# Optimization experiments

Measured on AMD Instinct MI355X. Metric: run time of the kernel, lower is better.

Reference implementation:

```python
import jax, jax.numpy as jnp
import numpy as np

B, N, D, H = 4, 4096, 128, 8
DH = D // H
EPS = 1e-6


def _layernorm(x, g, b):
    mu = jnp.mean(x, axis=-1, keepdims=True)
    var = jnp.var(x, axis=-1, keepdims=True)
    return (x - mu) * jax.lax.rsqrt(var + EPS) * g + b


def setup_inputs() -> dict:
    key = jax.random.key(0)
    ks = jax.random.split(key, 12)
    p = lambda k, shape: (jax.random.normal(k, shape, jnp.float32) * 0.02)
    x = jax.random.normal(ks[0], (B, N, D), jnp.float32)
    # scale fx so the sigmoid of the N-length contraction is not fully saturated
    fx = jax.random.normal(ks[1], (B, N, D), jnp.float32) / N
    return {
        "x": x,
        "fx": fx,
        "ln1_g": jnp.ones((D,), jnp.float32),
        "ln1_b": jnp.zeros((D,), jnp.float32),
        "wq": p(ks[2], (D, D)),
        "wk": p(ks[3], (D, D)),
        "wv": p(ks[4], (D, D)),
        "wo": p(ks[5], (D, D)),
        "bo": jnp.zeros((D,), jnp.float32),
        "ln2_g": jnp.ones((D,), jnp.float32),
        "ln2_b": jnp.zeros((D,), jnp.float32),
        "w1": p(ks[6], (D, D)),
        "b1": jnp.zeros((D,), jnp.float32),
        "w2": p(ks[7], (D, D)),
        "b2": jnp.zeros((D,), jnp.float32),
    }


def reference(x, fx, ln1_g, ln1_b, wq, wk, wv, wo, bo, ln2_g, ln2_b, w1, b1, w2, b2):
    b, n, d = x.shape
    h, dh = H, d // H
    # --- pre-norm linear self-attention ---
    xn = _layernorm(x, ln1_g, ln1_b)
    def heads(w):  # [b,n,d] @ w^T -> [b,h,n,dh]
        return jnp.einsum('bnd,ed->bne', xn, w).reshape(b, n, h, dh).transpose(0, 2, 1, 3)
    q = jax.nn.softmax(heads(wq), axis=-1)   # softmax over feature dim
    k = jax.nn.softmax(heads(wk), axis=2)    # softmax over sequence dim
    v = heads(wv)
    ctx = jnp.einsum('bhnd,bhne->bhde', k, v)         # [b,h,dh,dh]
    attn = jnp.einsum('bhnd,bhde->bhne', q, ctx)       # [b,h,n,dh]
    attn = attn.transpose(0, 2, 1, 3).reshape(b, n, d)
    attn = jnp.einsum('bnd,ed->bne', attn, wo) + bo
    x = x + attn                                       # residual (dropout=identity)
    # --- pre-norm MLP ---
    y = _layernorm(x, ln2_g, ln2_b)
    y = jax.nn.gelu(jnp.einsum('bnd,ed->bne', y, w1) + b1, approximate=False)
    y = jnp.einsum('bnd,ed->bne', y, w2) + b2
    x = x + y
    # --- quadratic update: sigmoid((x x^T) fx), as written in the module ---
    gram = jnp.einsum('bnd,bmd->bnm', x, x)            # [b,n,n] materialized, faithful
    fx = jax.nn.sigmoid(jnp.einsum('bnm,bmd->bnd', gram, fx))
    return (x, fx)
```

## Files before the change

### kernel.cpp

```cpp
#include <hip/hip_runtime.h>
#include <math.h>

#define BB 4
#define NN 4096
#define DD 128
#define MM (BB*NN)

typedef __attribute__((ext_vector_type(8))) short short8;
typedef __attribute__((ext_vector_type(4))) float f32x4;

__device__ inline short f2bf(float f) {
    unsigned u = __float_as_uint(f);
    u = (u + 0x7FFFu + ((u >> 16) & 1u)) >> 16;
    return (short)u;
}
__device__ inline float bf2f(short s) {
    return __uint_as_float(((unsigned)(unsigned short)s) << 16);
}
__device__ inline short8 pack_bf8(float4 a, float4 b) {
    short8 o;
    o[0] = f2bf(a.x); o[1] = f2bf(a.y); o[2] = f2bf(a.z); o[3] = f2bf(a.w);
    o[4] = f2bf(b.x); o[5] = f2bf(b.y); o[6] = f2bf(b.z); o[7] = f2bf(b.w);
    return o;
}
__device__ inline int swzoff(int row, int col) {
    return ((row * 128 + col) * 2) ^ ((row & 7) << 4);
}

__global__ __launch_bounds__(256) void wprep(const float* __restrict__ w0, const float* __restrict__ w1,
                                             const float* __restrict__ w2, const float* __restrict__ w3,
                                             const float* __restrict__ w4, short* __restrict__ wf) {
    int m = blockIdx.x >> 3;
    int j = (blockIdx.x & 7) * 256 + threadIdx.x;
    const float* W = (m == 0) ? w0 : (m == 1) ? w1 : (m == 2) ? w2 : (m == 3) ? w3 : w4;
    int nt = j >> 8, ks = (j >> 6) & 3, l = j & 63, r = l & 15, g = l >> 4;
    const float* src = W + (size_t)(nt * 16 + r) * DD + 32 * ks + 8 * g;
    float4 a = *(const float4*)src;
    float4 b = *(const float4*)(src + 4);
    ((short8*)(wf + (size_t)m * 16384))[j] = pack_bf8(a, b);
}

__global__ __launch_bounds__(256) void lnctx(const float* __restrict__ x,
                                             const float* __restrict__ lng,
                                             const float* __restrict__ lnb,
                                             const short* __restrict__ wf,
                                             float* __restrict__ partC,
                                             float* __restrict__ pcs) {
    __shared__ float ekL[32][132];
    __shared__ float vL[32][132];
    int t = threadIdx.x;
    int block_row = blockIdx.x * 32;
    int w = t >> 6, l = t & 63, r = l & 15, g = l >> 4;
    int rh = w >> 1, nt0 = (w & 1) << 2;
    int row0 = block_row + rh * 16;

    const float* ap = x + (size_t)(row0 + r) * DD + 8 * g;
    float4 av0[4], av1[4];
    #pragma unroll
    for (int ks = 0; ks < 4; ks++) {
        av0[ks] = *(const float4*)(ap + 32 * ks);
        av1[ks] = *(const float4*)(ap + 32 * ks + 4);
    }
    float s = 0.f, ss = 0.f;
    #pragma unroll
    for (int ks = 0; ks < 4; ks++) {
        float4 a = av0[ks], b = av1[ks];
        s  += a.x + a.y + a.z + a.w + b.x + b.y + b.z + b.w;
        ss += a.x*a.x + a.y*a.y + a.z*a.z + a.w*a.w + b.x*b.x + b.y*b.y + b.z*b.z + b.w*b.w;
    }
    s  += __shfl_xor(s, 16);  s  += __shfl_xor(s, 32);
    ss += __shfl_xor(ss, 16); ss += __shfl_xor(ss, 32);
    float mu = s * (1.0f / DD);
    float var = ss * (1.0f / DD) - mu * mu;
    float rs = rsqrtf(var + 1e-6f);

    short8 af[4];
    #pragma unroll
    for (int ks = 0; ks < 4; ks++) {
        float4 g0 = *(const float4*)(lng + 32 * ks + 8 * g);
        float4 g1 = *(const float4*)(lng + 32 * ks + 8 * g + 4);
        float4 b0 = *(const float4*)(lnb + 32 * ks + 8 * g);
        float4 b1 = *(const float4*)(lnb + 32 * ks + 8 * g + 4);
        float4 n0, n1;
        n0.x = (av0[ks].x - mu) * rs * g0.x + b0.x;
        n0.y = (av0[ks].y - mu) * rs * g0.y + b0.y;
        n0.z = (av0[ks].z - mu) * rs * g0.z + b0.z;
        n0.w = (av0[ks].w - mu) * rs * g0.w + b0.w;
        n1.x = (av1[ks].x - mu) * rs * g1.x + b1.x;
        n1.y = (av1[ks].y - mu) * rs * g1.y + b1.y;
        n1.z = (av1[ks].z - mu) * rs * g1.z + b1.z;
        n1.w = (av1[ks].w - mu) * rs * g1.w + b1.w;
        af[ks] = pack_bf8(n0, n1);
    }

    f32x4 acc[2][4];
    #pragma unroll
    for (int m = 0; m < 2; m++)
        #pragma unroll
        for (int n = 0; n < 4; n++) acc[m][n] = (f32x4){0.f, 0.f, 0.f, 0.f};
    const short8* wp8 = (const short8*)wf;
    #pragma unroll
    for (int ks = 0; ks < 4; ks++)
        #pragma unroll
        for (int m = 0; m < 2; m++)
            #pragma unroll
            for (int n = 0; n < 4; n++)
                acc[m][n] = __builtin_amdgcn_mfma_f32_16x16x32_bf16(
                    af[ks], wp8[(size_t)m * 2048 + ((nt0 + n) * 4 + ks) * 64 + l], acc[m][n], 0, 0, 0);

    #pragma unroll
    for (int n = 0; n < 4; n++) {
        int col = (nt0 + n) * 16 + r;
        #pragma unroll
        for (int j = 0; j < 4; j++) {
            int rowL = rh * 16 + 4 * g + j;
            ekL[rowL][col] = __expf(acc[0][n][j]);
            vL[rowL][col]  = acc[1][n][j];
        }
    }
    __syncthreads();

    int h = t >> 5, sub = t & 31, d = sub >> 1, e0 = (sub & 1) * 8;
    float cs = 0.f;
    float sc[8] = {0.f, 0.f, 0.f, 0.f, 0.f, 0.f, 0.f, 0.f};
    #pragma unroll 8
    for (int row = 0; row < 32; row++) {
        float ekv = ekL[row][h * 16 + d];
        float4 v0 = *(const float4*)&vL[row][h * 16 + e0];
        float4 v1 = *(const float4*)&vL[row][h * 16 + e0 + 4];
        sc[0] += ekv * v0.x; sc[1] += ekv * v0.y; sc[2] += ekv * v0.z; sc[3] += ekv * v0.w;
        sc[4] += ekv * v1.x; sc[5] += ekv * v1.y; sc[6] += ekv * v1.z; sc[7] += ekv * v1.w;
        cs += ekv;
    }
    float* cb = partC + (size_t)blockIdx.x * 2048 + h * 256 + d * 16 + e0;
    *(float4*)cb       = (float4){sc[0], sc[1], sc[2], sc[3]};
    *(float4*)(cb + 4) = (float4){sc[4], sc[5], sc[6], sc[7]};
    if ((sub & 1) == 0) pcs[(size_t)blockIdx.x * 128 + h * 16 + d] = cs;
}

__global__ __launch_bounds__(256) void ctxred(const float* __restrict__ part,
                                              float* __restrict__ ctxacc) {
    int k = blockIdx.x;
    int b = k >> 4, s0 = (k & 15) * 128;
    int t = threadIdx.x;
    int slot = s0 + (t & 127), half = t >> 7;
    float s = 0.f;
    #pragma unroll 8
    for (int c = half * 64; c < half * 64 + 64; c++)
        s += part[(size_t)((b << 7) + c) * 2048 + slot];
    __shared__ float red[128];
    if (half) red[t & 127] = s;
    __syncthreads();
    if (!half) ctxacc[(size_t)b * 2048 + slot] = s + red[t & 127];
}

__global__ __launch_bounds__(256) void build_mt_k(const float* __restrict__ ctxacc,
                                                  const float* __restrict__ pcs,
                                                  const float* __restrict__ wo,
                                                  short* __restrict__ mtfrag) {
    int b = blockIdx.x >> 3, nt = blockIdx.x & 7;
    int t = threadIdx.x;
    __shared__ float ctxL[2048];
    __shared__ float csL[128];
    __shared__ float woL[2048];
    #pragma unroll
    for (int i = 0; i < 8; i++) {
        int idx = i * 256 + t;
        ctxL[idx] = ctxacc[(size_t)b * 2048 + idx];
        woL[idx]  = wo[(size_t)(nt * 16) * DD + idx];
    }
    if (t < 128) {
        float s = 0.f;
        #pragma unroll 8
        for (int c = 0; c < 128; c++) s += pcs[(size_t)(b * 128 + c) * 128 + t];
        csL[t] = s;
    }
    __syncthreads();
    int ks = (t >> 6) & 3, l = t & 63, r = l & 15, g = l >> 4;
    short8 o;
    #pragma unroll
    for (int i2 = 0; i2 < 8; i2++) {
        int k = 32 * ks + 8 * g + i2;
        float inv = 1.0f / csL[k];
        const float* wrow = woL + r * DD + (k >> 4) * 16;
        float s = 0.f;
        #pragma unroll
        for (int eo = 0; eo < 16; eo++) s += ctxL[k * 16 + eo] * wrow[eo];
        o[i2] = f2bf(s * inv);
    }
    ((short8*)(mtfrag + (size_t)b * 16384))[nt * 256 + t] = o;
}

__global__ __launch_bounds__(256) void fused_mid(const float* __restrict__ x,
                                                 const float* __restrict__ ln1g,
                                                 const float* __restrict__ ln1b,
                                                 const short* __restrict__ wqf,
                                                 const short* __restrict__ mtf,
                                                 const float* __restrict__ bo,
                                                 const float* __restrict__ ln2g,
                                                 const float* __restrict__ ln2b,
                                                 const short* __restrict__ w1f,
                                                 const float* __restrict__ b1,
                                                 const short* __restrict__ w2f,
                                                 const float* __restrict__ b2,
                                                 float* __restrict__ xfinal,
                                                 short* __restrict__ xbf) {
    __shared__ __align__(16) char ex[32 * 128 * 2];
    __shared__ float ex2f[32][132];
    __shared__ float redS[4][16], redSS[4][16];
    int t = threadIdx.x;
    int block_row = blockIdx.x * 32;
    int w = t >> 6, l = t & 63, r = l & 15, g = l >> 4;
    int rh = w >> 1, nt0 = (w & 1) << 2;
    int row0 = block_row + rh * 16;
    int rrow = rh * 16 + r;

    const float* ap = x + (size_t)(row0 + r) * DD + 8 * g;
    float4 av0[4], av1[4];
    #pragma unroll
    for (int ks = 0; ks < 4; ks++) {
        av0[ks] = *(const float4*)(ap + 32 * ks);
        av1[ks] = *(const float4*)(ap + 32 * ks + 4);
    }
    if ((w & 1) == 0) {
        #pragma unroll
        for (int ks = 0; ks < 4; ks++) {
            *(float4*)&ex2f[rrow][32 * ks + 8 * g]     = av0[ks];
            *(float4*)&ex2f[rrow][32 * ks + 8 * g + 4] = av1[ks];
        }
    }
    float s = 0.f, ss = 0.f;
    #pragma unroll
    for (int ks = 0; ks < 4; ks++) {
        float4 a = av0[ks], b = av1[ks];
        s  += a.x + a.y + a.z + a.w + b.x + b.y + b.z + b.w;
        ss += a.x*a.x + a.y*a.y + a.z*a.z + a.w*a.w + b.x*b.x + b.y*b.y + b.z*b.z + b.w*b.w;
    }
    s  += __shfl_xor(s, 16);  s  += __shfl_xor(s, 32);
    ss += __shfl_xor(ss, 16); ss += __shfl_xor(ss, 32);
    float mu1 = s * (1.0f / DD);
    float var1 = ss * (1.0f / DD) - mu1 * mu1;
    float rs1 = rsqrtf(var1 + 1e-6f);
    short8 af[4];
    #pragma unroll
    for (int ks = 0; ks < 4; ks++) {
        float4 g0 = *(const float4*)(ln1g + 32 * ks + 8 * g);
        float4 g1 = *(const float4*)(ln1g + 32 * ks + 8 * g + 4);
        float4 b0 = *(const float4*)(ln1b + 32 * ks + 8 * g);
        float4 b1v = *(const float4*)(ln1b + 32 * ks + 8 * g + 4);
        float4 n0, n1;
        n0.x = (av0[ks].x - mu1) * rs1 * g0.x + b0.x;
        n0.y = (av0[ks].y - mu1) * rs1 * g0.y + b0.y;
        n0.z = (av0[ks].z - mu1) * rs1 * g0.z + b0.z;
        n0.w = (av0[ks].w - mu1) * rs1 * g0.w + b0.w;
        n1.x = (av1[ks].x - mu1) * rs1 * g1.x + b1v.x;
        n1.y = (av1[ks].y - mu1) * rs1 * g1.y + b1v.y;
        n1.z = (av1[ks].z - mu1) * rs1 * g1.z + b1v.z;
        n1.w = (av1[ks].w - mu1) * rs1 * g1.w + b1v.w;
        af[ks] = pack_bf8(n0, n1);
    }

    const short8* qp = (const short8*)wqf;
    f32x4 accq[4];
    #pragma unroll
    for (int n = 0; n < 4; n++) accq[n] = (f32x4){0.f, 0.f, 0.f, 0.f};
    #pragma unroll
    for (int ks = 0; ks < 4; ks++)
        #pragma unroll
        for (int n = 0; n < 4; n++)
            accq[n] = __builtin_amdgcn_mfma_f32_16x16x32_bf16(
                af[ks], qp[((nt0 + n) * 4 + ks) * 64 + l], accq[n], 0, 0, 0);
    #pragma unroll
    for (int n = 0; n < 4; n++) {
        int col = (nt0 + n) * 16 + r;
        #pragma unroll
        for (int j = 0; j < 4; j++) {
            float e = __expf(accq[n][j]);
            float sm = e;
            sm += __shfl_xor(sm, 1); sm += __shfl_xor(sm, 2);
            sm += __shfl_xor(sm, 4); sm += __shfl_xor(sm, 8);
            *(short*)(ex + swzoff(rh * 16 + 4 * g + j, col)) = f2bf(e / sm);
        }
    }
    __syncthreads();

    short8 qf[4];
    #pragma unroll
    for (int ks = 0; ks < 4; ks++)
        qf[ks] = *(const short8*)(ex + swzoff(rrow, 32 * ks + 8 * g));
    float xres[4][4];
    #pragma unroll
    for (int n = 0; n < 4; n++)
        #pragma unroll
        for (int j = 0; j < 4; j++)
            xres[n][j] = ex2f[rh * 16 + 4 * g + j][(nt0 + n) * 16 + r];

    const short8* mp = (const short8*)(mtf + (size_t)(block_row >> 12) * 16384);
    f32x4 acc[4];
    #pragma unroll
    for (int n = 0; n < 4; n++) acc[n] = (f32x4){0.f, 0.f, 0.f, 0.f};
    #pragma unroll
    for (int ks = 0; ks < 4; ks++)
        #pragma unroll
        for (int n = 0; n < 4; n++)
            acc[n] = __builtin_amdgcn_mfma_f32_16x16x32_bf16(
                qf[ks], mp[((nt0 + n) * 4 + ks) * 64 + l], acc[n], 0, 0, 0);

    float vv[4][4];
    #pragma unroll
    for (int n = 0; n < 4; n++) {
        int col = (nt0 + n) * 16 + r;
        float bv = bo[col];
        #pragma unroll
        for (int j = 0; j < 4; j++)
            vv[n][j] = acc[n][j] + bv + xres[n][j];
    }

    #pragma unroll
    for (int j = 0; j < 4; j++) {
        float s1  = vv[0][j] + vv[1][j] + vv[2][j] + vv[3][j];
        float s2 = vv[0][j]*vv[0][j] + vv[1][j]*vv[1][j] + vv[2][j]*vv[2][j] + vv[3][j]*vv[3][j];
        s1 += __shfl_xor(s1, 1); s1 += __shfl_xor(s1, 2); s1 += __shfl_xor(s1, 4); s1 += __shfl_xor(s1, 8);
        s2 += __shfl_xor(s2, 1); s2 += __shfl_xor(s2, 2); s2 += __shfl_xor(s2, 4); s2 += __shfl_xor(s2, 8);
        if (r == 0) { redS[w][4 * g + j] = s1; redSS[w][4 * g + j] = s2; }
    }
    __syncthreads();
    int base = w & 2;
    #pragma unroll
    for (int j = 0; j < 4; j++) {
        int rr = 4 * g + j;
        float S  = redS[base][rr]  + redS[base + 1][rr];
        float SS = redSS[base][rr] + redSS[base + 1][rr];
        float mu = S * (1.0f / DD);
        float var = SS * (1.0f / DD) - mu * mu;
        float rs = rsqrtf(var + 1e-6f);
        int rowL = rh * 16 + rr;
        #pragma unroll
        for (int n = 0; n < 4; n++) {
            int col = (nt0 + n) * 16 + r;
            float y = (vv[n][j] - mu) * rs * ln2g[col] + ln2b[col];
            *(short*)(ex + swzoff(rowL, col)) = f2bf(y);
        }
    }
    __syncthreads();
    short8 yf[4];
    #pragma unroll
    for (int ks = 0; ks < 4; ks++)
        yf[ks] = *(const short8*)(ex + swzoff(rrow, 32 * ks + 8 * g));
    __syncthreads();
    const short8* w1p = (const short8*)w1f;
    f32x4 acc2[4];
    #pragma unroll
    for (int n = 0; n < 4; n++) acc2[n] = (f32x4){0.f, 0.f, 0.f, 0.f};
    #pragma unroll
    for (int ks = 0; ks < 4; ks++)
        #pragma unroll
        for (int n = 0; n < 4; n++)
            acc2[n] = __builtin_amdgcn_mfma_f32_16x16x32_bf16(
                yf[ks], w1p[((nt0 + n) * 4 + ks) * 64 + l], acc2[n], 0, 0, 0);
    #pragma unroll
    for (int n = 0; n < 4; n++) {
        int col = (nt0 + n) * 16 + r;
        float bv = b1[col];
        #pragma unroll
        for (int j = 0; j < 4; j++) {
            float v = acc2[n][j] + bv;
            v = 0.5f * v * (1.0f + erff(v * 0.70710678118654752f));
            *(short*)(ex + swzoff(rh * 16 + 4 * g + j, col)) = f2bf(v);
        }
    }
    __syncthreads();
    short8 hf[4];
    #pragma unroll
    for (int ks = 0; ks < 4; ks++)
        hf[ks] = *(const short8*)(ex + swzoff(rrow, 32 * ks + 8 * g));
    const short8* w2p = (const short8*)w2f;
    f32x4 acc3[4];
    #pragma unroll
    for (int n = 0; n < 4; n++) acc3[n] = (f32x4){0.f, 0.f, 0.f, 0.f};
    #pragma unroll
    for (int ks = 0; ks < 4; ks++)
        #pragma unroll
        for (int n = 0; n < 4; n++)
            acc3[n] = __builtin_amdgcn_mfma_f32_16x16x32_bf16(
                hf[ks], w2p[((nt0 + n) * 4 + ks) * 64 + l], acc3[n], 0, 0, 0);
    #pragma unroll
    for (int n = 0; n < 4; n++) {
        int col = (nt0 + n) * 16 + r;
        float bv = b2[col];
        #pragma unroll
        for (int j = 0; j < 4; j++) {
            float v = acc3[n][j] + bv + vv[n][j];
            size_t row = (size_t)(row0 + 4 * g + j);
            xfinal[row * DD + col] = v;
            xbf[row * DD + col] = f2bf(v);
        }
    }
}

__global__ __launch_bounds__(512) void sbuild_p(const short* __restrict__ xf,
                                                const float* __restrict__ fx,
                                                short* __restrict__ part) {
    int b = blockIdx.x >> 6, chunk = blockIdx.x & 63;
    int t = threadIdx.x;
    __shared__ float xs[64 * 128], fs[64 * 128];
    const short* xb = xf + ((size_t)b * NN + chunk * 64) * DD;
    const float* fb = fx + ((size_t)b * NN + chunk * 64) * DD;
    const short8* xg = (const short8*)xb;
    float4* xs4 = (float4*)xs; float4* fs4 = (float4*)fs;
    const float4* fg = (const float4*)fb;
    #pragma unroll
    for (int i = 0; i < 2; i++) {
        int j = i * 512 + t;
        short8 s8 = xg[j];
        float4 a = {bf2f(s8[0]), bf2f(s8[1]), bf2f(s8[2]), bf2f(s8[3])};
        float4 c = {bf2f(s8[4]), bf2f(s8[5]), bf2f(s8[6]), bf2f(s8[7])};
        xs4[2 * j] = a; xs4[2 * j + 1] = c;
    }
    #pragma unroll
    for (int i = 0; i < 4; i++) {
        int j = i * 512 + t;
        fs4[j] = fg[j];
    }
    __syncthreads();
    int td = t & 15, te = t >> 4;
    float acc[8][4];
    #pragma unroll
    for (int a = 0; a < 8; a++)
        #pragma unroll
        for (int c = 0; c < 4; c++) acc[a][c] = 0.f;
    for (int r = 0; r < 64; r++) {
        float4 x0 = xs4[r * 32 + td * 2], x1 = xs4[r * 32 + td * 2 + 1];
        float4 f0 = fs4[r * 32 + te];
        float xv[8] = {x0.x, x0.y, x0.z, x0.w, x1.x, x1.y, x1.z, x1.w};
        float fv[4] = {f0.x, f0.y, f0.z, f0.w};
        #pragma unroll
        for (int a = 0; a < 8; a++)
            #pragma unroll
            for (int c = 0; c < 4; c++) acc[a][c] = fmaf(xv[a], fv[c], acc[a][c]);
    }
    short* pb = part + (size_t)blockIdx.x * 16384;
    #pragma unroll
    for (int ci = 0; ci < 4; ci++) {
        short8 o;
        #pragma unroll
        for (int a = 0; a < 8; a++) o[a] = f2bf(acc[a][ci]);
        *(short8*)(pb + (size_t)(te * 4 + ci) * 128 + td * 8) = o;
    }
}

__global__ __launch_bounds__(256) void sreduce2(const short* __restrict__ part,
                                                float* __restrict__ S_T) {
    int b = blockIdx.x >> 7, e = blockIdx.x & 127;
    int t = threadIdx.x;
    int d8 = (t & 15) * 8;
    int ch0 = t >> 4;
    float s[8] = {0.f, 0.f, 0.f, 0.f, 0.f, 0.f, 0.f, 0.f};
    #pragma unroll
    for (int cc = 0; cc < 4; cc++) {
        int ch = ch0 + cc * 16;
        short8 u = *(const short8*)(part + (size_t)(b * 64 + ch) * 16384 + e * 128 + d8);
        #pragma unroll
        for (int i = 0; i < 8; i++) s[i] += bf2f(u[i]);
    }
    #pragma unroll
    for (int i = 0; i < 8; i++) {
        s[i] += __shfl_xor(s[i], 16);
        s[i] += __shfl_xor(s[i], 32);
    }
    __shared__ float red[4][128];
    int w = t >> 6;
    if ((t & 63) < 16) {
        #pragma unroll
        for (int i = 0; i < 8; i++) red[w][d8 + i] = s[i];
    }
    __syncthreads();
    if (t < 128)
        S_T[((size_t)b * 128 + e) * 128 + t] = red[0][t] + red[1][t] + red[2][t] + red[3][t];
}

__global__ __launch_bounds__(256) void gemm_sig(const short* __restrict__ A,
                                                const float* __restrict__ S_T,
                                                float* __restrict__ Cf) {
    int t = threadIdx.x;
    int block_row = blockIdx.x * 32;
    int w = t >> 6, l = t & 63, r = l & 15, g = l >> 4;
    int row0 = block_row + ((w >> 1) << 4);
    int nt0 = (w & 1) << 2;
    const short8* ap = (const short8*)(A + (size_t)(row0 + r) * DD + 8 * g);
    short8 af[4];
    #pragma unroll
    for (int ks = 0; ks < 4; ks++) af[ks] = ap[ks * 4];
    const float* sp = S_T + (size_t)(block_row >> 12) * 16384;
    short8 bf[4][4];
    #pragma unroll
    for (int n = 0; n < 4; n++) {
        const float* se = sp + (size_t)((nt0 + n) * 16 + r) * 128 + 8 * g;
        #pragma unroll
        for (int ks = 0; ks < 4; ks++) {
            float4 a = *(const float4*)(se + 32 * ks);
            float4 c = *(const float4*)(se + 32 * ks + 4);
            bf[n][ks] = pack_bf8(a, c);
        }
    }
    f32x4 acc[4];
    #pragma unroll
    for (int n = 0; n < 4; n++) acc[n] = (f32x4){0.f, 0.f, 0.f, 0.f};
    #pragma unroll
    for (int ks = 0; ks < 4; ks++)
        #pragma unroll
        for (int n = 0; n < 4; n++)
            acc[n] = __builtin_amdgcn_mfma_f32_16x16x32_bf16(
                af[ks], bf[n][ks], acc[n], 0, 0, 0);
    #pragma unroll
    for (int n = 0; n < 4; n++) {
        int col = (nt0 + n) * 16 + r;
        #pragma unroll
        for (int j = 0; j < 4; j++) {
            float v = 1.0f / (1.0f + __expf(-acc[n][j]));
            Cf[(size_t)(row0 + 4 * g + j) * DD + col] = v;
        }
    }
}

extern "C" void kernel_launch(void* const* d_in, const int* in_sizes, int n_in,
                              void* d_out, int out_size, void* d_ws, size_t ws_size,
                              hipStream_t stream) {
    const float* x    = (const float*)d_in[0];
    const float* fx   = (const float*)d_in[1];
    const float* ln1g = (const float*)d_in[2];
    const float* ln1b = (const float*)d_in[3];
    const float* wq   = (const float*)d_in[4];
    const float* wk   = (const float*)d_in[5];
    const float* wv   = (const float*)d_in[6];
    const float* wo   = (const float*)d_in[7];
    const float* bo   = (const float*)d_in[8];
    const float* ln2g = (const float*)d_in[9];
    const float* ln2b = (const float*)d_in[10];
    const float* w1   = (const float*)d_in[11];
    const float* b1   = (const float*)d_in[12];
    const float* w2   = (const float*)d_in[13];
    const float* b2   = (const float*)d_in[14];

    float* out = (float*)d_out;
    float* xfinal = out;
    float* fxout  = out + (size_t)MM * DD;

    float* ws = (float*)d_ws;
    short* xbf    = (short*)ws;
    short* partSb = (short*)(ws + 1048576);
    short* wfW    = (short*)(ws + 3145728);
    float* partC  = ws + 3145728 + 40960;
    float* pcs    = partC + 1048576;
    float* ctxacc = pcs + 65536;
    float* S_T    = ctxacc + 8192;
    short* mtf    = (short*)(S_T + 65536);

    wprep<<<40, 256, 0, stream>>>(wq, wk, wv, w1, w2, wfW);
    lnctx<<<512, 256, 0, stream>>>(x, ln1g, ln1b, wfW + 16384, partC, pcs);
    ctxred<<<64, 256, 0, stream>>>(partC, ctxacc);
    build_mt_k<<<32, 256, 0, stream>>>(ctxacc, pcs, wo, mtf);
    fused_mid<<<512, 256, 0, stream>>>(x, ln1g, ln1b, wfW, mtf, bo, ln2g, ln2b,
                                       wfW + 3 * 16384, b1, wfW + 4 * 16384, b2,
                                       xfinal, xbf);
    sbuild_p<<<256, 512, 0, stream>>>(xbf, fx, partSb);
    sreduce2<<<512, 256, 0, stream>>>(partSb, S_T);
    gemm_sig<<<512, 256, 0, stream>>>(xbf, S_T, fxout);
}
```

Before: 73.06 us.

## Halve row tile to 16 rows per block, doubling grid size for lnctx, fused_mid, gemm_sig

Shrinks the per-block row tile from 32 to 16 rows, so each of the four waves now covers two column tiles of the same 16 rows instead of four column tiles of half the rows. Grids double to 1024 blocks to give more parallelism on the large CU count. The partial-context buffers double in size, so ctxred and build_mt_k must reduce twice as many partials. In exchange, weight fragments are reloaded by twice as many blocks and the LayerNorm statistics in fused_mid now need a four-wave cross reduction.

```diff
diff --git a/kernel.cpp b/kernel.cpp
--- a/kernel.cpp
+++ b/kernel.cpp
@@ -46,15 +46,14 @@
                                              const short* __restrict__ wf,
                                              float* __restrict__ partC,
                                              float* __restrict__ pcs) {
-    __shared__ float ekL[32][132];
-    __shared__ float vL[32][132];
-    int t = threadIdx.x;
-    int block_row = blockIdx.x * 32;
+    __shared__ float ekL[16][132];
+    __shared__ float vL[16][132];
+    int t = threadIdx.x;
+    int block_row = blockIdx.x * 16;
     int w = t >> 6, l = t & 63, r = l & 15, g = l >> 4;
-    int rh = w >> 1, nt0 = (w & 1) << 2;
-    int row0 = block_row + rh * 16;
-
-    const float* ap = x + (size_t)(row0 + r) * DD + 8 * g;
+    int nt0 = w << 1;
+
+    const float* ap = x + (size_t)(block_row + r) * DD + 8 * g;
     float4 av0[4], av1[4];
     #pragma unroll
     for (int ks = 0; ks < 4; ks++) {
@@ -93,27 +92,27 @@
         af[ks] = pack_bf8(n0, n1);
     }
 
-    f32x4 acc[2][4];
+    f32x4 acc[2][2];
     #pragma unroll
     for (int m = 0; m < 2; m++)
         #pragma unroll
-        for (int n = 0; n < 4; n++) acc[m][n] = (f32x4){0.f, 0.f, 0.f, 0.f};
+        for (int n = 0; n < 2; n++) acc[m][n] = (f32x4){0.f, 0.f, 0.f, 0.f};
     const short8* wp8 = (const short8*)wf;
     #pragma unroll
     for (int ks = 0; ks < 4; ks++)
         #pragma unroll
         for (int m = 0; m < 2; m++)
             #pragma unroll
-            for (int n = 0; n < 4; n++)
+            for (int n = 0; n < 2; n++)
                 acc[m][n] = __builtin_amdgcn_mfma_f32_16x16x32_bf16(
                     af[ks], wp8[(size_t)m * 2048 + ((nt0 + n) * 4 + ks) * 64 + l], acc[m][n], 0, 0, 0);
 
     #pragma unroll
-    for (int n = 0; n < 4; n++) {
+    for (int n = 0; n < 2; n++) {
         int col = (nt0 + n) * 16 + r;
         #pragma unroll
         for (int j = 0; j < 4; j++) {
-            int rowL = rh * 16 + 4 * g + j;
+            int rowL = 4 * g + j;
             ekL[rowL][col] = __expf(acc[0][n][j]);
             vL[rowL][col]  = acc[1][n][j];
         }
@@ -123,8 +122,8 @@
     int h = t >> 5, sub = t & 31, d = sub >> 1, e0 = (sub & 1) * 8;
     float cs = 0.f;
     float sc[8] = {0.f, 0.f, 0.f, 0.f, 0.f, 0.f, 0.f, 0.f};
-    #pragma unroll 8
-    for (int row = 0; row < 32; row++) {
+    #pragma unroll
+    for (int row = 0; row < 16; row++) {
         float ekv = ekL[row][h * 16 + d];
         float4 v0 = *(const float4*)&vL[row][h * 16 + e0];
         float4 v1 = *(const float4*)&vL[row][h * 16 + e0 + 4];
@@ -146,8 +145,8 @@
     int slot = s0 + (t & 127), half = t >> 7;
     float s = 0.f;
     #pragma unroll 8
-    for (int c = half * 64; c < half * 64 + 64; c++)
-        s += part[(size_t)((b << 7) + c) * 2048 + slot];
+    for (int c = half * 128; c < half * 128 + 128; c++)
+        s += part[(size_t)(b * 256 + c) * 2048 + slot];
     __shared__ float red[128];
     if (half) red[t & 127] = s;
     __syncthreads();
@@ -172,7 +171,7 @@
     if (t < 128) {
         float s = 0.f;
         #pragma unroll 8
-        for (int c = 0; c < 128; c++) s += pcs[(size_t)(b * 128 + c) * 128 + t];
+        for (int c = 0; c < 256; c++) s += pcs[(size_t)(b * 256 + c) * 128 + t];
         csL[t] = s;
     }
     __syncthreads();
@@ -205,28 +204,26 @@
                                                  const float* __restrict__ b2,
                                                  float* __restrict__ xfinal,
                                                  short* __restrict__ xbf) {
-    __shared__ __align__(16) char ex[32 * 128 * 2];
-    __shared__ float ex2f[32][132];
+    __shared__ __align__(16) char ex[16 * 128 * 2];
+    __shared__ float ex2f[16][132];
     __shared__ float redS[4][16], redSS[4][16];
     int t = threadIdx.x;
-    int block_row = blockIdx.x * 32;
+    int block_row = blockIdx.x * 16;
     int w = t >> 6, l = t & 63, r = l & 15, g = l >> 4;
-    int rh = w >> 1, nt0 = (w & 1) << 2;
-    int row0 = block_row + rh * 16;
-    int rrow = rh * 16 + r;
-
-    const float* ap = x + (size_t)(row0 + r) * DD + 8 * g;
+    int nt0 = w << 1;
+
+    const float* ap = x + (size_t)(block_row + r) * DD + 8 * g;
     float4 av0[4], av1[4];
     #pragma unroll
     for (int ks = 0; ks < 4; ks++) {
         av0[ks] = *(const float4*)(ap + 32 * ks);
         av1[ks] = *(const float4*)(ap + 32 * ks + 4);
     }
-    if ((w & 1) == 0) {
+    if (w == 0) {
         #pragma unroll
         for (int ks = 0; ks < 4; ks++) {
-            *(float4*)&ex2f[rrow][32 * ks + 8 * g]     = av0[ks];
-            *(float4*)&ex2f[rrow][32 * ks + 8 * g + 4] = av1[ks];
+            *(float4*)&ex2f[r][32 * ks + 8 * g]     = av0[ks];
+            *(float4*)&ex2f[r][32 * ks + 8 * g + 4] = av1[ks];
         }
     }
     float s = 0.f, ss = 0.f;
@@ -261,17 +258,17 @@
     }
 
     const short8* qp = (const short8*)wqf;
-    f32x4 accq[4];
-    #pragma unroll
-    for (int n = 0; n < 4; n++) accq[n] = (f32x4){0.f, 0.f, 0.f, 0.f};
-    #pragma unroll
-    for (int ks = 0; ks < 4; ks++)
-        #pragma unroll
-        for (int n = 0; n < 4; n++)
+    f32x4 accq[2];
+    #pragma unroll
+    for (int n = 0; n < 2; n++) accq[n] = (f32x4){0.f, 0.f, 0.f, 0.f};
+    #pragma unroll
+    for (int ks = 0; ks < 4; ks++)
+        #pragma unroll
+        for (int n = 0; n < 2; n++)
             accq[n] = __builtin_amdgcn_mfma_f32_16x16x32_bf16(
                 af[ks], qp[((nt0 + n) * 4 + ks) * 64 + l], accq[n], 0, 0, 0);
     #pragma unroll
-    for (int n = 0; n < 4; n++) {
+    for (int n = 0; n < 2; n++) {
         int col = (nt0 + n) * 16 + r;
         #pragma unroll
         for (int j = 0; j < 4; j++) {
@@ -279,7 +276,7 @@
             float sm = e;
             sm += __shfl_xor(sm, 1); sm += __shfl_xor(sm, 2);
             sm += __shfl_xor(sm, 4); sm += __shfl_xor(sm, 8);
-            *(short*)(ex + swzoff(rh * 16 + 4 * g + j, col)) = f2bf(e / sm);
+            *(short*)(ex + swzoff(4 * g + j, col)) = f2bf(e / sm);
         }
     }
     __syncthreads();
@@ -287,28 +284,28 @@
     short8 qf[4];
     #pragma unroll
     for (int ks = 0; ks < 4; ks++)
-        qf[ks] = *(const short8*)(ex + swzoff(rrow, 32 * ks + 8 * g));
-    float xres[4][4];
-    #pragma unroll
-    for (int n = 0; n < 4; n++)
+        qf[ks] = *(const short8*)(ex + swzoff(r, 32 * ks + 8 * g));
+    float xres[2][4];
+    #pragma unroll
+    for (int n = 0; n < 2; n++)
         #pragma unroll
         for (int j = 0; j < 4; j++)
-            xres[n][j] = ex2f[rh * 16 + 4 * g + j][(nt0 + n) * 16 + r];
+            xres[n][j] = ex2f[4 * g + j][(nt0 + n) * 16 + r];
 
     const short8* mp = (const short8*)(mtf + (size_t)(block_row >> 12) * 16384);
-    f32x4 acc[4];
-    #pragma unroll
-    for (int n = 0; n < 4; n++) acc[n] = (f32x4){0.f, 0.f, 0.f, 0.f};
-    #pragma unroll
-    for (int ks = 0; ks < 4; ks++)
-        #pragma unroll
-        for (int n = 0; n < 4; n++)
+    f32x4 acc[2];
+    #pragma unroll
+    for (int n = 0; n < 2; n++) acc[n] = (f32x4){0.f, 0.f, 0.f, 0.f};
+    #pragma unroll
+    for (int ks = 0; ks < 4; ks++)
+        #pragma unroll
+        for (int n = 0; n < 2; n++)
             acc[n] = __builtin_amdgcn_mfma_f32_16x16x32_bf16(
                 qf[ks], mp[((nt0 + n) * 4 + ks) * 64 + l], acc[n], 0, 0, 0);
 
-    float vv[4][4];
-    #pragma unroll
-    for (int n = 0; n < 4; n++) {
+    float vv[2][4];
+    #pragma unroll
+    for (int n = 0; n < 2; n++) {
         int col = (nt0 + n) * 16 + r;
         float bv = bo[col];
         #pragma unroll
@@ -318,80 +315,78 @@
 
     #pragma unroll
     for (int j = 0; j < 4; j++) {
-        float s1  = vv[0][j] + vv[1][j] + vv[2][j] + vv[3][j];
-        float s2 = vv[0][j]*vv[0][j] + vv[1][j]*vv[1][j] + vv[2][j]*vv[2][j] + vv[3][j]*vv[3][j];
+        float s1 = vv[0][j] + vv[1][j];
+        float s2 = vv[0][j]*vv[0][j] + vv[1][j]*vv[1][j];
         s1 += __shfl_xor(s1, 1); s1 += __shfl_xor(s1, 2); s1 += __shfl_xor(s1, 4); s1 += __shfl_xor(s1, 8);
         s2 += __shfl_xor(s2, 1); s2 += __shfl_xor(s2, 2); s2 += __shfl_xor(s2, 4); s2 += __shfl_xor(s2, 8);
         if (r == 0) { redS[w][4 * g + j] = s1; redSS[w][4 * g + j] = s2; }
     }
     __syncthreads();
-    int base = w & 2;
     #pragma unroll
     for (int j = 0; j < 4; j++) {
         int rr = 4 * g + j;
-        float S  = redS[base][rr]  + redS[base + 1][rr];
-        float SS = redSS[base][rr] + redSS[base + 1][rr];
+        float S  = redS[0][rr]  + redS[1][rr]  + redS[2][rr]  + redS[3][rr];
+        float SS = redSS[0][rr] + redSS[1][rr] + redSS[2][rr] + redSS[3][rr];
         float mu = S * (1.0f / DD);
         float var = SS * (1.0f / DD) - mu * mu;
         float rs = rsqrtf(var + 1e-6f);
-        int rowL = rh * 16 + rr;
-        #pragma unroll
-        for (int n = 0; n < 4; n++) {
+        #pragma unroll
+        for (int n = 0; n < 2; n++) {
             int col = (nt0 + n) * 16 + r;
             float y = (vv[n][j] - mu) * rs * ln2g[col] + ln2b[col];
-            *(short*)(ex + swzoff(rowL, col)) = f2bf(y);
+            *(short*)(ex + swzoff(rr, col)) = f2bf(y);
         }
     }
     __syncthreads();
     short8 yf[4];
     #pragma unroll
     for (int ks = 0; ks < 4; ks++)
-        yf[ks] = *(const short8*)(ex + swzoff(rrow, 32 * ks + 8 * g));
+        yf[ks] = *(const short8*)(ex + swzoff(r, 32 * ks + 8 * g));
     __syncthreads();
     const short8* w1p = (const short8*)w1f;
-    f32x4 acc2[4];
-    #pragma unroll
-    for (int n = 0; n < 4; n++) acc2[n] = (f32x4){0.f, 0.f, 0.f, 0.f};
-    #pragma unroll
-    for (int ks = 0; ks < 4; ks++)
-        #pragma unroll
-        for (int n = 0; n < 4; n++)
+    f32x4 acc2[2];
+    #pragma unroll
+    for (int n = 0; n < 2; n++) acc2[n] = (f32x4){0.f, 0.f, 0.f, 0.f};
+    #pragma unroll
+    for (int ks = 0; ks < 4; ks++)
+        #pragma unroll
+        for (int n = 0; n < 2; n++)
             acc2[n] = __builtin_amdgcn_mfma_f32_16x16x32_bf16(
                 yf[ks], w1p[((nt0 + n) * 4 + ks) * 64 + l], acc2[n], 0, 0, 0);
     #pragma unroll
-    for (int n = 0; n < 4; n++) {
+    for (int n = 0; n < 2; n++) {
         int col = (nt0 + n) * 16 + r;
         float bv = b1[col];
         #pragma unroll
         for (int j = 0; j < 4; j++) {
             float v = acc2[n][j] + bv;
             v = 0.5f * v * (1.0f + erff(v * 0.70710678118654752f));
-            *(short*)(ex + swzoff(rh * 16 + 4 * g + j, col)) = f2bf(v);
+            *(short*)(ex + swzoff(4 * g + j, col)) = f2bf(v);
         }
     }
     __syncthreads();
     short8 hf[4];
     #pragma unroll
     for (int ks = 0; ks < 4; ks++)
-        hf[ks] = *(const short8*)(ex + swzoff(rrow, 32 * ks + 8 * g));
+        hf[ks] = *(const short8*)(ex + swzoff(r, 32 * ks + 8 * g));
     const short8* w2p = (const short8*)w2f;
-    f32x4 acc3[4];
-    #pragma unroll
-    for (int n = 0; n < 4; n++) acc3[n] = (f32x4){0.f, 0.f, 0.f, 0.f};
-    #pragma unroll
-    for (int ks = 0; ks < 4; ks++)
-        #pragma unroll
-        for (int n = 0; n < 4; n++)
+    f32x4 acc3[2];
+    #pragma unroll
+    for (int n = 0; n < 2; n++) acc3[n] = (f32x4){0.f, 0.f, 0.f, 0.f};
+    #pragma unroll
+    for (int ks = 0; ks < 4; ks++)
+        #pragma unroll
+        for (int n = 0; n < 2; n++)
             acc3[n] = __builtin_amdgcn_mfma_f32_16x16x32_bf16(
                 hf[ks], w2p[((nt0 + n) * 4 + ks) * 64 + l], acc3[n], 0, 0, 0);
     #pragma unroll
-    for (int n = 0; n < 4; n++) {
+    for (int n = 0; n < 2; n++) {
         int col = (nt0 + n) * 16 + r;
         float bv = b2[col];
         #pragma unroll
         for (int j = 0; j < 4; j++) {
             float v = acc3[n][j] + bv + vv[n][j];
-            size_t row = (size_t)(row0 + 4 * g + j);
+            size_t row = (size_t)(block_row + 4 * g + j);
             xfinal[row * DD + col] = v;
             xbf[row * DD + col] = f2bf(v);
         }
@@ -483,18 +478,17 @@
                                                 const float* __restrict__ S_T,
                                                 float* __restrict__ Cf) {
     int t = threadIdx.x;
-    int block_row = blockIdx.x * 32;
+    int block_row = blockIdx.x * 16;
     int w = t >> 6, l = t & 63, r = l & 15, g = l >> 4;
-    int row0 = block_row + ((w >> 1) << 4);
-    int nt0 = (w & 1) << 2;
-    const short8* ap = (const short8*)(A + (size_t)(row0 + r) * DD + 8 * g);
+    int nt0 = w << 1;
+    const short8* ap = (const short8*)(A + (size_t)(block_row + r) * DD + 8 * g);
     short8 af[4];
     #pragma unroll
     for (int ks = 0; ks < 4; ks++) af[ks] = ap[ks * 4];
     const float* sp = S_T + (size_t)(block_row >> 12) * 16384;
-    short8 bf[4][4];
-    #pragma unroll
-    for (int n = 0; n < 4; n++) {
+    short8 bf[2][4];
+    #pragma unroll
+    for (int n = 0; n < 2; n++) {
         const float* se = sp + (size_t)((nt0 + n) * 16 + r) * 128 + 8 * g;
         #pragma unroll
         for (int ks = 0; ks < 4; ks++) {
@@ -503,22 +497,22 @@
             bf[n][ks] = pack_bf8(a, c);
         }
     }
-    f32x4 acc[4];
-    #pragma unroll
-    for (int n = 0; n < 4; n++) acc[n] = (f32x4){0.f, 0.f, 0.f, 0.f};
-    #pragma unroll
-    for (int ks = 0; ks < 4; ks++)
-        #pragma unroll
-        for (int n = 0; n < 4; n++)
+    f32x4 acc[2];
+    #pragma unroll
+    for (int n = 0; n < 2; n++) acc[n] = (f32x4){0.f, 0.f, 0.f, 0.f};
+    #pragma unroll
+    for (int ks = 0; ks < 4; ks++)
+        #pragma unroll
+        for (int n = 0; n < 2; n++)
             acc[n] = __builtin_amdgcn_mfma_f32_16x16x32_bf16(
                 af[ks], bf[n][ks], acc[n], 0, 0, 0);
     #pragma unroll
-    for (int n = 0; n < 4; n++) {
+    for (int n = 0; n < 2; n++) {
         int col = (nt0 + n) * 16 + r;
         #pragma unroll
         for (int j = 0; j < 4; j++) {
             float v = 1.0f / (1.0f + __expf(-acc[n][j]));
-            Cf[(size_t)(row0 + 4 * g + j) * DD + col] = v;
+            Cf[(size_t)(block_row + 4 * g + j) * DD + col] = v;
         }
     }
 }
@@ -551,19 +545,19 @@
     short* partSb = (short*)(ws + 1048576);
     short* wfW    = (short*)(ws + 3145728);
     float* partC  = ws + 3145728 + 40960;
-    float* pcs    = partC + 1048576;
-    float* ctxacc = pcs + 65536;
+    float* pcs    = partC + 2097152;
+    float* ctxacc = pcs + 131072;
     float* S_T    = ctxacc + 8192;
     short* mtf    = (short*)(S_T + 65536);
 
     wprep<<<40, 256, 0, stream>>>(wq, wk, wv, w1, w2, wfW);
-    lnctx<<<512, 256, 0, stream>>>(x, ln1g, ln1b, wfW + 16384, partC, pcs);
+    lnctx<<<1024, 256, 0, stream>>>(x, ln1g, ln1b, wfW + 16384, partC, pcs);
     ctxred<<<64, 256, 0, stream>>>(partC, ctxacc);
     build_mt_k<<<32, 256, 0, stream>>>(ctxacc, pcs, wo, mtf);
-    fused_mid<<<512, 256, 0, stream>>>(x, ln1g, ln1b, wfW, mtf, bo, ln2g, ln2b,
-                                       wfW + 3 * 16384, b1, wfW + 4 * 16384, b2,
-                                       xfinal, xbf);
+    fused_mid<<<1024, 256, 0, stream>>>(x, ln1g, ln1b, wfW, mtf, bo, ln2g, ln2b,
+                                        wfW + 3 * 16384, b1, wfW + 4 * 16384, b2,
+                                        xfinal, xbf);
     sbuild_p<<<256, 512, 0, stream>>>(xbf, fx, partSb);
     sreduce2<<<512, 256, 0, stream>>>(partSb, S_T);
-    gemm_sig<<<512, 256, 0, stream>>>(xbf, S_T, fxout);
-}
+    gemm_sig<<<1024, 256, 0, stream>>>(xbf, S_T, fxout);
+}
```

Result: slower. 83.62 us (+14.5%).

## Restructure fused_mid to one wave per 16-row tile computing all columns

Applied to the files above, without the earlier changes.

Changes fused_mid from 4-wave blocks over 32 rows, each wave covering half of the output columns, to single-wave blocks over 16 rows that compute all 128 columns. The cross-wave LayerNorm reduction through shared memory and its barrier go away because the row statistics now come entirely from intra-wave shuffles. Each wave does twice the MFMA work and holds twice the accumulators, which raises register pressure. The grid becomes 1024 blocks of 64 threads, and each wave now loads the full weight fragments itself.

```diff
diff --git a/kernel.cpp b/kernel.cpp
--- a/kernel.cpp
+++ b/kernel.cpp
@@ -191,29 +191,25 @@
     ((short8*)(mtfrag + (size_t)b * 16384))[nt * 256 + t] = o;
 }
 
-__global__ __launch_bounds__(256) void fused_mid(const float* __restrict__ x,
-                                                 const float* __restrict__ ln1g,
-                                                 const float* __restrict__ ln1b,
-                                                 const short* __restrict__ wqf,
-                                                 const short* __restrict__ mtf,
-                                                 const float* __restrict__ bo,
-                                                 const float* __restrict__ ln2g,
-                                                 const float* __restrict__ ln2b,
-                                                 const short* __restrict__ w1f,
-                                                 const float* __restrict__ b1,
-                                                 const short* __restrict__ w2f,
-                                                 const float* __restrict__ b2,
-                                                 float* __restrict__ xfinal,
-                                                 short* __restrict__ xbf) {
-    __shared__ __align__(16) char ex[32 * 128 * 2];
-    __shared__ float ex2f[32][132];
-    __shared__ float redS[4][16], redSS[4][16];
-    int t = threadIdx.x;
-    int block_row = blockIdx.x * 32;
-    int w = t >> 6, l = t & 63, r = l & 15, g = l >> 4;
-    int rh = w >> 1, nt0 = (w & 1) << 2;
-    int row0 = block_row + rh * 16;
-    int rrow = rh * 16 + r;
+__global__ __launch_bounds__(64) void fused_mid(const float* __restrict__ x,
+                                                const float* __restrict__ ln1g,
+                                                const float* __restrict__ ln1b,
+                                                const short* __restrict__ wqf,
+                                                const short* __restrict__ mtf,
+                                                const float* __restrict__ bo,
+                                                const float* __restrict__ ln2g,
+                                                const float* __restrict__ ln2b,
+                                                const short* __restrict__ w1f,
+                                                const float* __restrict__ b1,
+                                                const short* __restrict__ w2f,
+                                                const float* __restrict__ b2,
+                                                float* __restrict__ xfinal,
+                                                short* __restrict__ xbf) {
+    __shared__ __align__(16) char ex[16 * 128 * 2];
+    __shared__ float ex2f[16][132];
+    int l = threadIdx.x;
+    int row0 = blockIdx.x * 16;
+    int r = l & 15, g = l >> 4;
 
     const float* ap = x + (size_t)(row0 + r) * DD + 8 * g;
     float4 av0[4], av1[4];
@@ -221,13 +217,8 @@
     for (int ks = 0; ks < 4; ks++) {
         av0[ks] = *(const float4*)(ap + 32 * ks);
         av1[ks] = *(const float4*)(ap + 32 * ks + 4);
-    }
-    if ((w & 1) == 0) {
-        #pragma unroll
-        for (int ks = 0; ks < 4; ks++) {
-            *(float4*)&ex2f[rrow][32 * ks + 8 * g]     = av0[ks];
-            *(float4*)&ex2f[rrow][32 * ks + 8 * g + 4] = av1[ks];
-        }
+        *(float4*)&ex2f[r][32 * ks + 8 * g]     = av0[ks];
+        *(float4*)&ex2f[r][32 * ks + 8 * g + 4] = av1[ks];
     }
     float s = 0.f, ss = 0.f;
     #pragma unroll
@@ -261,25 +252,25 @@
     }
 
     const short8* qp = (const short8*)wqf;
-    f32x4 accq[4];
-    #pragma unroll
-    for (int n = 0; n < 4; n++) accq[n] = (f32x4){0.f, 0.f, 0.f, 0.f};
-    #pragma unroll
-    for (int ks = 0; ks < 4; ks++)
-        #pragma unroll
-        for (int n = 0; n < 4; n++)
+    f32x4 accq[8];
+    #pragma unroll
+    for (int n = 0; n < 8; n++) accq[n] = (f32x4){0.f, 0.f, 0.f, 0.f};
+    #pragma unroll
+    for (int ks = 0; ks < 4; ks++)
+        #pragma unroll
+        for (int n = 0; n < 8; n++)
             accq[n] = __builtin_amdgcn_mfma_f32_16x16x32_bf16(
-                af[ks], qp[((nt0 + n) * 4 + ks) * 64 + l], accq[n], 0, 0, 0);
-    #pragma unroll
-    for (int n = 0; n < 4; n++) {
-        int col = (nt0 + n) * 16 + r;
+                af[ks], qp[(n * 4 + ks) * 64 + l], accq[n], 0, 0, 0);
+    #pragma unroll
+    for (int n = 0; n < 8; n++) {
+        int col = n * 16 + r;
         #pragma unroll
         for (int j = 0; j < 4; j++) {
             float e = __expf(accq[n][j]);
             float sm = e;
             sm += __shfl_xor(sm, 1); sm += __shfl_xor(sm, 2);
             sm += __shfl_xor(sm, 4); sm += __shfl_xor(sm, 8);
-            *(short*)(ex + swzoff(rh * 16 + 4 * g + j, col)) = f2bf(e / sm);
+            *(short*)(ex + swzoff(4 * g + j, col)) = f2bf(e / sm);
         }
     }
     __syncthreads();
@@ -287,106 +278,93 @@
     short8 qf[4];
     #pragma unroll
     for (int ks = 0; ks < 4; ks++)
-        qf[ks] = *(const short8*)(ex + swzoff(rrow, 32 * ks + 8 * g));
-    float xres[4][4];
-    #pragma unroll
-    for (int n = 0; n < 4; n++)
+        qf[ks] = *(const short8*)(ex + swzoff(r, 32 * ks + 8 * g));
+
+    const short8* mp = (const short8*)(mtf + (size_t)(row0 >> 12) * 16384);
+    f32x4 acc[8];
+    #pragma unroll
+    for (int n = 0; n < 8; n++) acc[n] = (f32x4){0.f, 0.f, 0.f, 0.f};
+    #pragma unroll
+    for (int ks = 0; ks < 4; ks++)
+        #pragma unroll
+        for (int n = 0; n < 8; n++)
+            acc[n] = __builtin_amdgcn_mfma_f32_16x16x32_bf16(
+                qf[ks], mp[(n * 4 + ks) * 64 + l], acc[n], 0, 0, 0);
+
+    float vv[8][4];
+    #pragma unroll
+    for (int n = 0; n < 8; n++) {
+        int col = n * 16 + r;
+        float bv = bo[col];
         #pragma unroll
         for (int j = 0; j < 4; j++)
-            xres[n][j] = ex2f[rh * 16 + 4 * g + j][(nt0 + n) * 16 + r];
-
-    const short8* mp = (const short8*)(mtf + (size_t)(block_row >> 12) * 16384);
-    f32x4 acc[4];
-    #pragma unroll
-    for (int n = 0; n < 4; n++) acc[n] = (f32x4){0.f, 0.f, 0.f, 0.f};
-    #pragma unroll
-    for (int ks = 0; ks < 4; ks++)
-        #pragma unroll
-        for (int n = 0; n < 4; n++)
-            acc[n] = __builtin_amdgcn_mfma_f32_16x16x32_bf16(
-                qf[ks], mp[((nt0 + n) * 4 + ks) * 64 + l], acc[n], 0, 0, 0);
-
-    float vv[4][4];
-    #pragma unroll
-    for (int n = 0; n < 4; n++) {
-        int col = (nt0 + n) * 16 + r;
-        float bv = bo[col];
-        #pragma unroll
-        for (int j = 0; j < 4; j++)
-            vv[n][j] = acc[n][j] + bv + xres[n][j];
+            vv[n][j] = acc[n][j] + bv + ex2f[4 * g + j][col];
     }
 
     #pragma unroll
     for (int j = 0; j < 4; j++) {
-        float s1  = vv[0][j] + vv[1][j] + vv[2][j] + vv[3][j];
-        float s2 = vv[0][j]*vv[0][j] + vv[1][j]*vv[1][j] + vv[2][j]*vv[2][j] + vv[3][j]*vv[3][j];
+        float s1 = 0.f, s2 = 0.f;
+        #pragma unroll
+        for (int n = 0; n < 8; n++) { s1 += vv[n][j]; s2 += vv[n][j] * vv[n][j]; }
         s1 += __shfl_xor(s1, 1); s1 += __shfl_xor(s1, 2); s1 += __shfl_xor(s1, 4); s1 += __shfl_xor(s1, 8);
         s2 += __shfl_xor(s2, 1); s2 += __shfl_xor(s2, 2); s2 += __shfl_xor(s2, 4); s2 += __shfl_xor(s2, 8);
-        if (r == 0) { redS[w][4 * g + j] = s1; redSS[w][4 * g + j] = s2; }
-    }
-    __syncthreads();
-    int base = w & 2;
-    #pragma unroll
-    for (int j = 0; j < 4; j++) {
-        int rr = 4 * g + j;
-        float S  = redS[base][rr]  + redS[base + 1][rr];
-        float SS = redSS[base][rr] + redSS[base + 1][rr];
-        float mu = S * (1.0f / DD);
-        float var = SS * (1.0f / DD) - mu * mu;
+        float mu = s1 * (1.0f / DD);
+        float var = s2 * (1.0f / DD) - mu * mu;
         float rs = rsqrtf(var + 1e-6f);
-        int rowL = rh * 16 + rr;
-        #pragma unroll
-        for (int n = 0; n < 4; n++) {
-            int col = (nt0 + n) * 16 + r;
+        #pragma unroll
+        for (int n = 0; n < 8; n++) {
+            int col = n * 16 + r;
             float y = (vv[n][j] - mu) * rs * ln2g[col] + ln2b[col];
-            *(short*)(ex + swzoff(rowL, col)) = f2bf(y);
+            *(short*)(ex + swzoff(4 * g + j, col)) = f2bf(y);
         }
     }
     __syncthreads();
     short8 yf[4];
     #pragma unroll
     for (int ks = 0; ks < 4; ks++)
-        yf[ks] = *(const short8*)(ex + swzoff(rrow, 32 * ks + 8 * g));
-    __syncthreads();
+        yf[ks] = *(const short8*)(ex + swzoff(r, 32 * ks + 8 * g));
+    __syncthreads();
+
     const short8* w1p = (const short8*)w1f;
-    f32x4 acc2[4];
-    #pragma unroll
-    for (int n = 0; n < 4; n++) acc2[n] = (f32x4){0.f, 0.f, 0.f, 0.f};
-    #pragma unroll
-    for (int ks = 0; ks < 4; ks++)
-        #pragma unroll
-        for (int n = 0; n < 4; n++)
+    f32x4 acc2[8];
+    #pragma unroll
+    for (int n = 0; n < 8; n++) acc2[n] = (f32x4){0.f, 0.f, 0.f, 0.f};
+    #pragma unroll
+    for (int ks = 0; ks < 4; ks++)
+        #pragma unroll
+        for (int n = 0; n < 8; n++)
             acc2[n] = __builtin_amdgcn_mfma_f32_16x16x32_bf16(
-                yf[ks], w1p[((nt0 + n) * 4 + ks) * 64 + l], acc2[n], 0, 0, 0);
-    #pragma unroll
-    for (int n = 0; n < 4; n++) {
-        int col = (nt0 + n) * 16 + r;
+                yf[ks], w1p[(n * 4 + ks) * 64 + l], acc2[n], 0, 0, 0);
+    #pragma unroll
+    for (int n = 0; n < 8; n++) {
+        int col = n * 16 + r;
         float bv = b1[col];
         #pragma unroll
         for (int j = 0; j < 4; j++) {
             float v = acc2[n][j] + bv;
             v = 0.5f * v * (1.0f + erff(v * 0.70710678118654752f));
-            *(short*)(ex + swzoff(rh * 16 + 4 * g + j, col)) = f2bf(v);
+            *(short*)(ex + swzoff(4 * g + j, col)) = f2bf(v);
         }
     }
     __syncthreads();
     short8 hf[4];
     #pragma unroll
     for (int ks = 0; ks < 4; ks++)
-        hf[ks] = *(const short8*)(ex + swzoff(rrow, 32 * ks + 8 * g));
+        hf[ks] = *(const short8*)(ex + swzoff(r, 32 * ks + 8 * g));
+
     const short8* w2p = (const short8*)w2f;
-    f32x4 acc3[4];
-    #pragma unroll
-    for (int n = 0; n < 4; n++) acc3[n] = (f32x4){0.f, 0.f, 0.f, 0.f};
-    #pragma unroll
-    for (int ks = 0; ks < 4; ks++)
-        #pragma unroll
-        for (int n = 0; n < 4; n++)
+    f32x4 acc3[8];
+    #pragma unroll
+    for (int n = 0; n < 8; n++) acc3[n] = (f32x4){0.f, 0.f, 0.f, 0.f};
+    #pragma unroll
+    for (int ks = 0; ks < 4; ks++)
+        #pragma unroll
+        for (int n = 0; n < 8; n++)
             acc3[n] = __builtin_amdgcn_mfma_f32_16x16x32_bf16(
-                hf[ks], w2p[((nt0 + n) * 4 + ks) * 64 + l], acc3[n], 0, 0, 0);
-    #pragma unroll
-    for (int n = 0; n < 4; n++) {
-        int col = (nt0 + n) * 16 + r;
+                hf[ks], w2p[(n * 4 + ks) * 64 + l], acc3[n], 0, 0, 0);
+    #pragma unroll
+    for (int n = 0; n < 8; n++) {
+        int col = n * 16 + r;
         float bv = b2[col];
         #pragma unroll
         for (int j = 0; j < 4; j++) {
@@ -560,7 +538,7 @@
     lnctx<<<512, 256, 0, stream>>>(x, ln1g, ln1b, wfW + 16384, partC, pcs);
     ctxred<<<64, 256, 0, stream>>>(partC, ctxacc);
     build_mt_k<<<32, 256, 0, stream>>>(ctxacc, pcs, wo, mtf);
-    fused_mid<<<512, 256, 0, stream>>>(x, ln1g, ln1b, wfW, mtf, bo, ln2g, ln2b,
+    fused_mid<<<1024, 64, 0, stream>>>(x, ln1g, ln1b, wfW, mtf, bo, ln2g, ln2b,
                                        wfW + 3 * 16384, b1, wfW + 4 * 16384, b2,
                                        xfinal, xbf);
     sbuild_p<<<256, 512, 0, stream>>>(xbf, fx, partSb);
```

After: 80.58 us. +10.3%, slower.
